# Kernel tuning notes

Measured on AMD Instinct MI355X. Metric: run time of the kernel, lower is better.

The kernel has to match this reference:

```python
import jax, jax.numpy as jnp
import numpy as np

B, C_L_IN, C_L_OUT, C_J = 512, 64, 64, 16


def setup_inputs() -> dict:
    key = jax.random.key(0)
    ks = jax.random.split(key, 8)
    std = 0.02 / C_L_IN ** 0.5
    return {
        "F_in": jax.random.normal(ks[0], (B, C_L_IN, 4, 4), jnp.float32),
        "theta": jax.random.normal(ks[1], (B, C_J), jnp.float32),
        "W_bias": std * jax.random.normal(ks[2], (C_L_OUT, C_L_IN, 4, 4), jnp.float32),
        "W_cos": std * jax.random.normal(ks[3], (C_L_OUT, C_L_IN, C_J, 4, 4), jnp.float32),
        "W_sin": std * jax.random.normal(ks[4], (C_L_OUT, C_L_IN, C_J, 4, 4), jnp.float32),
        "Wb_bias": std * jax.random.normal(ks[5], (C_L_OUT, C_L_IN, 4, 4), jnp.float32),
        "Wb_cos": std * jax.random.normal(ks[6], (C_L_OUT, C_L_IN, C_J, 4, 4), jnp.float32),
        "Wb_sin": std * jax.random.normal(ks[7], (C_L_OUT, C_L_IN, C_J, 4, 4), jnp.float32),
    }


def reference(F_in, theta, W_bias, W_cos, W_sin, Wb_bias, Wb_cos, Wb_sin):
    cos_t = jnp.cos(theta)  # (B, C_J)
    sin_t = jnp.sin(theta)
    # U, Ub: (B, C_L_out, C_L_in, 4, 4)
    U = (W_bias
         + jnp.einsum('jicpq,bc->bjipq', W_cos, cos_t)
         + jnp.einsum('jicpq,bc->bjipq', W_sin, sin_t))
    Ub = (Wb_bias
          + jnp.einsum('jicpq,bc->bjipq', Wb_cos, cos_t)
          + jnp.einsum('jicpq,bc->bjipq', Wb_sin, sin_t))
    term1 = jnp.einsum('bipq,bjiqr->bjpr', F_in, U)
    term2 = jnp.einsum('bjipq,biqr->bjpr', Ub, F_in)
    return term1 + term2
```

## Files before the change

### kernel.cpp

```cpp
#include <hip/hip_runtime.h>


#define NRO_B   512
#define NRO_CL  64
#define K_DIM   8448
#define M_DIM   2048
#define N_DIM   256
#define SK      8
#define B_ELems  ((size_t)N_DIM * K_DIM)
#define FV_ELems ((size_t)M_DIM * N_DIM)
#define P_ELems  ((size_t)2 * SK * M_DIM * N_DIM)

typedef __attribute__((ext_vector_type(8))) _Float16 half8;
typedef __attribute__((ext_vector_type(4))) _Float16 half4_t;
typedef __attribute__((ext_vector_type(4))) float floatx4;

__device__ __forceinline__ void load16(const float* p, float w[4][4]) {
    const float4* p4 = (const float4*)p;
    #pragma unroll
    for (int a = 0; a < 4; ++a) {
        float4 x = p4[a];
        w[a][0] = x.x; w[a][1] = x.y; w[a][2] = x.z; w[a][3] = x.w;
    }
}

__device__ __forceinline__ half8 scale8(half8 v, _Float16 s) {
    half8 r;
    #pragma unroll
    for (int x = 0; x < 8; ++x) r[x] = v[x] * s;
    return r;
}

__global__ __launch_bounds__(256) void nro_prep(
    const float* __restrict__ F_in,
    const float* __restrict__ W_bias, const float* __restrict__ W_cos,
    const float* __restrict__ W_sin,  const float* __restrict__ Wb_bias,
    const float* __restrict__ Wb_cos, const float* __restrict__ Wb_sin,
    _Float16* __restrict__ Bbuf,
    _Float16* __restrict__ Fv)
{
    const int w = threadIdx.x >> 6, i = threadIdx.x & 63;
    if (blockIdx.x < 128) {
        const int b = blockIdx.x * 4 + w;
        float f[4][4];
        load16(F_in + ((size_t)b * 64 + i) * 16, f);
        #pragma unroll
        for (int a = 0; a < 4; ++a) {
            half4_t v0 = { (_Float16)f[a][0], (_Float16)f[a][1],
                           (_Float16)f[a][2], (_Float16)f[a][3] };
            *(half4_t*)(Fv + (size_t)(b * 4 + a) * 256 + i * 4) = v0;
            half4_t v1 = { (_Float16)f[0][a], (_Float16)f[1][a],
                           (_Float16)f[2][a], (_Float16)f[3][a] };
            *(half4_t*)(Fv + FV_ELems + (size_t)(b * 4 + a) * 256 + i * 4) = v1;
        }
    } else {
        const int unit = (blockIdx.x - 128) * 4 + w;
        const int j = unit >> 5, c = (unit >> 1) & 15, h = unit & 1;
        _Float16* Bd = Bbuf + (size_t)h * B_ELems;
        const size_t wbase = (((size_t)(j * 64 + i)) * 16 + c) * 16;

        float wc4[4][4], ws4[4][4];
        if (h == 0) { load16(W_cos  + wbase, wc4); load16(W_sin  + wbase, ws4); }
        else        { load16(Wb_cos + wbase, wc4); load16(Wb_sin + wbase, ws4); }

        const int gc  = (1 + c)  * 8 + (i >> 3);
        const int gs  = (17 + c) * 8 + (i >> 3);
        const int kin = (i & 7) * 4;
        #pragma unroll
        for (int a = 0; a < 4; ++a) {
            const int n = j * 4 + a;
            half4_t vc, vs;
            if (h == 0) {
                vc = (half4_t){ (_Float16)wc4[0][a], (_Float16)wc4[1][a],
                                (_Float16)wc4[2][a], (_Float16)wc4[3][a] };
                vs = (half4_t){ (_Float16)ws4[0][a], (_Float16)ws4[1][a],
                                (_Float16)ws4[2][a], (_Float16)ws4[3][a] };
            } else {
                vc = (half4_t){ (_Float16)wc4[a][0], (_Float16)wc4[a][1],
                                (_Float16)wc4[a][2], (_Float16)wc4[a][3] };
                vs = (half4_t){ (_Float16)ws4[a][0], (_Float16)ws4[a][1],
                                (_Float16)ws4[a][2], (_Float16)ws4[a][3] };
            }
            *(half4_t*)(Bd + ((size_t)gc * 256 + n) * 32 + kin) = vc;
            *(half4_t*)(Bd + ((size_t)gs * 256 + n) * 32 + kin) = vs;
        }
        if (c == 0) {
            float t[4][4];
            load16(((h == 0) ? W_bias : Wb_bias) + ((size_t)(j * 64 + i)) * 16, t);
            #pragma unroll
            for (int a = 0; a < 4; ++a) {
                half4_t v;
                if (h == 0) v = (half4_t){ (_Float16)t[0][a], (_Float16)t[1][a],
                                           (_Float16)t[2][a], (_Float16)t[3][a] };
                else        v = (half4_t){ (_Float16)t[a][0], (_Float16)t[a][1],
                                           (_Float16)t[a][2], (_Float16)t[a][3] };
                *(half4_t*)(Bd + ((size_t)(i >> 3) * 256 + (j * 4 + a)) * 32 + kin) = v;
            }
        }
    }
}

__global__ __launch_bounds__(256, 2) void nro_gemm(
    const _Float16* __restrict__ Bbuf, const _Float16* __restrict__ Fv,
    const float* __restrict__ theta,
    float* __restrict__ part)
{
    const int zs = blockIdx.x;
    const int z  = zs >> 3;
    const int sk = zs & 7;
    const int m0 = blockIdx.y * 64;

    const _Float16* Bm = Bbuf + (size_t)z * B_ELems;
    const _Float16* Fm = Fv + (size_t)z * FV_ELems + (size_t)m0 * 256;

    __shared__ _Float16 Fs[64 * 264];
    __shared__ float    trig[16 * 34];

    const int tid  = threadIdx.x;
    const int lane = tid & 63;
    const int w    = tid >> 6;
    const int wn   = w * 64;

    #pragma unroll
    for (int kk = 0; kk < 8; ++kk) {
        const int idx = kk * 256 + tid;
        const int row = idx >> 5, cf = idx & 31;
        half8 v = *(const half8*)(Fm + (size_t)row * 256 + cf * 8);
        *(half8*)(Fs + row * 264 + cf * 8) = v;
    }
    {
        const int bl = tid >> 4, c = tid & 15;
        const float th = theta[(m0 >> 2) * 16 + tid];
        trig[bl * 34 + 1 + c]  = __cosf(th);
        trig[bl * 34 + 17 + c] = __sinf(th);
        if (c == 0) trig[bl * 34] = 1.0f;
    }
    __syncthreads();

    const int fr = lane & 15, fq8 = (lane >> 4) * 8;

    const _Float16* Brow[4];
    #pragma unroll
    for (int t = 0; t < 4; ++t)
        Brow[t] = Bm + (size_t)(wn + t * 16 + fr) * 32 + fq8;

    floatx4 acc[4][4] = {};
    _Float16 tv[4] = {};
    int cp_last = -1;

    const int base = sk * 33;
    half8 q0[4], q1[4];
    #pragma unroll
    for (int t = 0; t < 4; ++t) {
        q0[t] = *(const half8*)(Brow[t] + (size_t)(base + 0) * 8192);
        q1[t] = *(const half8*)(Brow[t] + (size_t)(base + 1) * 8192);
    }

    #define NRO_CHUNK(GABS, QREG)                                             \
        {                                                                     \
            const int cp_ = (GABS) >> 3;                                      \
            if (cp_ != cp_last) {                                             \
                cp_last = cp_;                                                \
                _Pragma("unroll")                                             \
                for (int t = 0; t < 4; ++t)                                   \
                    tv[t] = (_Float16)trig[(t * 4 + (fr >> 2)) * 34 + cp_];   \
            }                                                                 \
            const int iq0_ = ((GABS) & 7) * 32;                               \
            half8 af[4];                                                      \
            _Pragma("unroll")                                                 \
            for (int t = 0; t < 4; ++t) {                                     \
                half8 fvf = *(const half8*)(Fs + (t * 16 + fr) * 264          \
                                            + iq0_ + fq8);                    \
                af[t] = scale8(fvf, tv[t]);                                   \
            }                                                                 \
            _Pragma("unroll")                                                 \
            for (int mt = 0; mt < 4; ++mt)                                    \
                _Pragma("unroll")                                             \
                for (int nt = 0; nt < 4; ++nt)                                \
                    acc[mt][nt] = __builtin_amdgcn_mfma_f32_16x16x32_f16(     \
                        af[mt], QREG[nt], acc[mt][nt], 0, 0, 0);              \
        }

    for (int it = 0; it < 16; ++it) {
        const int c0 = base + 2 * it;
        half8 p0[4], p1[4];
        #pragma unroll
        for (int t = 0; t < 4; ++t)
            p0[t] = *(const half8*)(Brow[t] + (size_t)(c0 + 2) * 8192);
        if (it < 15) {
            #pragma unroll
            for (int t = 0; t < 4; ++t)
                p1[t] = *(const half8*)(Brow[t] + (size_t)(c0 + 3) * 8192);
        }
        NRO_CHUNK(c0, q0);
        NRO_CHUNK(c0 + 1, q1);
        #pragma unroll
        for (int t = 0; t < 4; ++t) q0[t] = p0[t];
        if (it < 15) {
            #pragma unroll
            for (int t = 0; t < 4; ++t) q1[t] = p1[t];
        }
    }
    NRO_CHUNK(base + 32, q0);
    #undef NRO_CHUNK

    const int col = lane & 15, row4 = (lane >> 4) * 4;
    #pragma unroll
    for (int mt = 0; mt < 4; ++mt)
        #pragma unroll
        for (int nt = 0; nt < 4; ++nt)
            #pragma unroll
            for (int e = 0; e < 4; ++e) {
                const int m = m0 + mt * 16 + row4 + e;
                const int n = wn + nt * 16 + col;
                part[((size_t)zs * M_DIM + m) * N_DIM + n] = acc[mt][nt][e];
            }
}

__global__ __launch_bounds__(256) void nro_reduce(
    const float* __restrict__ part, float* __restrict__ out)
{
    const int t = blockIdx.x * 256 + threadIdx.x;
    const int b = t >> 8;
    const int j = (t >> 2) & 63;
    const int p = t & 3;

    float4 o = make_float4(0.f, 0.f, 0.f, 0.f);
    #pragma unroll
    for (int sk = 0; sk < SK; ++sk) {
        const float4 c1 = *(const float4*)(
            part + ((size_t)sk * M_DIM + b * 4 + p) * N_DIM + j * 4);
        o.x += c1.x; o.y += c1.y; o.z += c1.z; o.w += c1.w;
        const float* p2 = part + ((size_t)(SK + sk) * M_DIM + b * 4) * N_DIM + j * 4 + p;
        o.x += p2[0 * N_DIM]; o.y += p2[1 * N_DIM];
        o.z += p2[2 * N_DIM]; o.w += p2[3 * N_DIM];
    }
    *(float4*)(out + ((size_t)(b * 64 + j) * 16 + p * 4)) = o;
}

__global__ __launch_bounds__(256, 2) void nro_fallback(
    const float* __restrict__ F_in, const float* __restrict__ theta,
    const float* __restrict__ W_bias, const float* __restrict__ W_cos,
    const float* __restrict__ W_sin,  const float* __restrict__ Wb_bias,
    const float* __restrict__ Wb_cos, const float* __restrict__ Wb_sin,
    float* __restrict__ out)
{
    __shared__ float smem[8448];
    const int j      = blockIdx.x >> 3;
    const int isplit = blockIdx.x & 7;
    const int i0     = isplit * 8;
    const int lane   = threadIdx.x & 63;
    const int chunk  = __builtin_amdgcn_readfirstlane(threadIdx.x >> 6);
    const int b      = blockIdx.y * 64 + lane;
    const int tid    = threadIdx.x;
    {
        float4* s4 = (float4*)smem;
        const int base16  = (j * 64 + i0) * 16;
        const int base256 = (j * 64 + i0) * 256;
        if (tid < 32)      s4[tid] = ((const float4*)(W_bias + base16))[tid];
        else if (tid < 64) s4[tid] = ((const float4*)(Wb_bias + base16))[tid - 32];
        #pragma unroll
        for (int r = 0; r < 2; ++r) {
            const int k = r * 256 + tid;
            s4[64 + k]   = ((const float4*)(W_cos  + base256))[k];
            s4[576 + k]  = ((const float4*)(W_sin  + base256))[k];
            s4[1088 + k] = ((const float4*)(Wb_cos + base256))[k];
            s4[1600 + k] = ((const float4*)(Wb_sin + base256))[k];
        }
    }
    float csc[16], css[16];
    #pragma unroll
    for (int c = 0; c < 16; ++c) {
        float t = theta[b * 16 + c];
        csc[c] = __cosf(t); css[c] = __sinf(t);
    }
    __syncthreads();
    float acc[16];
    #pragma unroll
    for (int e = 0; e < 16; ++e) acc[e] = 0.0f;
    #pragma unroll
    for (int ii = 0; ii < 2; ++ii) {
        const int il = chunk * 2 + ii;
        const int i  = i0 + il;
        float f[16];
        const float4* fp = (const float4*)(F_in + (b * 64 + i) * 16);
        #pragma unroll
        for (int v = 0; v < 4; ++v) {
            float4 x = fp[v];
            f[v*4+0]=x.x; f[v*4+1]=x.y; f[v*4+2]=x.z; f[v*4+3]=x.w;
        }
        const float* wb  = smem + il * 16;
        const float* wbb = smem + 128  + il * 16;
        const float* wc  = smem + 256  + il * 256;
        const float* wsn = smem + 2304 + il * 256;
        const float* wbc = smem + 4352 + il * 256;
        const float* wbs = smem + 6400 + il * 256;
        float U[16], Ub[16];
        #pragma unroll
        for (int e = 0; e < 16; ++e) { U[e] = wb[e]; Ub[e] = wbb[e]; }
        #pragma unroll 4
        for (int c = 0; c < 16; ++c) {
            const float cc = csc[c], ss = css[c];
            #pragma unroll
            for (int e = 0; e < 16; ++e) {
                U[e]  = fmaf(wc [c*16+e], cc, U[e]);
                U[e]  = fmaf(wsn[c*16+e], ss, U[e]);
                Ub[e] = fmaf(wbc[c*16+e], cc, Ub[e]);
                Ub[e] = fmaf(wbs[c*16+e], ss, Ub[e]);
            }
        }
        #pragma unroll
        for (int p = 0; p < 4; ++p)
            #pragma unroll
            for (int r = 0; r < 4; ++r) {
                float a = acc[p*4+r];
                #pragma unroll
                for (int q = 0; q < 4; ++q) {
                    a = fmaf(f[p*4+q],  U[q*4+r], a);
                    a = fmaf(Ub[p*4+q], f[q*4+r], a);
                }
                acc[p*4+r] = a;
            }
    }
    __syncthreads();
    if (chunk > 0) {
        float* r = smem + (chunk - 1) * 1088 + lane * 17;
        #pragma unroll
        for (int e = 0; e < 16; ++e) r[e] = acc[e];
    }
    __syncthreads();
    if (chunk == 0) {
        #pragma unroll
        for (int cc = 0; cc < 3; ++cc) {
            const float* r = smem + cc * 1088 + lane * 17;
            #pragma unroll
            for (int e = 0; e < 16; ++e) acc[e] += r[e];
        }
        float* o = out + ((size_t)b * 64 + j) * 16;
        #pragma unroll
        for (int e = 0; e < 16; ++e) atomicAdd(o + e, acc[e]);
    }
}

extern "C" void kernel_launch(void* const* d_in, const int* in_sizes, int n_in,
                              void* d_out, int out_size, void* d_ws, size_t ws_size,
                              hipStream_t stream) {
    const float* F_in    = (const float*)d_in[0];
    const float* theta   = (const float*)d_in[1];
    const float* W_bias  = (const float*)d_in[2];
    const float* W_cos   = (const float*)d_in[3];
    const float* W_sin   = (const float*)d_in[4];
    const float* Wb_bias = (const float*)d_in[5];
    const float* Wb_cos  = (const float*)d_in[6];
    const float* Wb_sin  = (const float*)d_in[7];
    float* out = (float*)d_out;

    const size_t needB  = 2 * B_ELems  * sizeof(_Float16);
    const size_t needFv = 2 * FV_ELems * sizeof(_Float16);
    const size_t needP  = P_ELems * sizeof(float);
    if (ws_size >= needB + needFv + needP) {
        _Float16* Bbuf = (_Float16*)d_ws;
        _Float16* Fv   = (_Float16*)((char*)d_ws + needB);
        float*    part = (float*)((char*)d_ws + needB + needFv);
        nro_prep<<<640, 256, 0, stream>>>(F_in, W_bias, W_cos, W_sin,
                                          Wb_bias, Wb_cos, Wb_sin, Bbuf, Fv);
        nro_gemm<<<dim3(16, 32), 256, 0, stream>>>(Bbuf, Fv, theta, part);
        nro_reduce<<<512, 256, 0, stream>>>(part, out);
    } else {
        hipMemsetAsync(out, 0, (size_t)out_size * sizeof(float), stream);
        dim3 grid(64 * 8, 512 / 64, 1);
        nro_fallback<<<grid, 256, 0, stream>>>(
            F_in, theta, W_bias, W_cos, W_sin, Wb_bias, Wb_cos, Wb_sin, out);
    }
}
```

Measured before the change: 110.2 us.

## Fuse split-K reduction into GEMM via last-block atomic counter

Removes the separate reduce kernel. Each GEMM block writes its partial tile, then bumps a per-row-block atomic counter, and the last of the 16 blocks sums all split-K partials and writes the output. The counters are zeroed in the prep kernel. This saves a kernel launch and lets the reduction overlap with other GEMM blocks, but the reduction now runs on only 32 blocks at the tail, which may serialize.

```diff
diff --git a/kernel.cpp b/kernel.cpp
--- a/kernel.cpp
+++ b/kernel.cpp
@@ -37,9 +37,11 @@
     const float* __restrict__ W_sin,  const float* __restrict__ Wb_bias,
     const float* __restrict__ Wb_cos, const float* __restrict__ Wb_sin,
     _Float16* __restrict__ Bbuf,
-    _Float16* __restrict__ Fv)
+    _Float16* __restrict__ Fv,
+    int* __restrict__ cnt)
 {
     const int w = threadIdx.x >> 6, i = threadIdx.x & 63;
+    if (blockIdx.x == 0 && threadIdx.x < 32) cnt[threadIdx.x] = 0;
     if (blockIdx.x < 128) {
         const int b = blockIdx.x * 4 + w;
         float f[4][4];
@@ -103,7 +105,9 @@
 __global__ __launch_bounds__(256, 2) void nro_gemm(
     const _Float16* __restrict__ Bbuf, const _Float16* __restrict__ Fv,
     const float* __restrict__ theta,
-    float* __restrict__ part)
+    float* __restrict__ part,
+    int* __restrict__ cnt,
+    float* __restrict__ out)
 {
     const int zs = blockIdx.x;
     const int z  = zs >> 3;
@@ -115,6 +119,7 @@
 
     __shared__ _Float16 Fs[64 * 264];
     __shared__ float    trig[16 * 34];
+    __shared__ int      s_old;
 
     const int tid  = threadIdx.x;
     const int lane = tid & 63;
@@ -204,38 +209,48 @@
     NRO_CHUNK(base + 32, q0);
     #undef NRO_CHUNK
 
-    const int col = lane & 15, row4 = (lane >> 4) * 4;
-    #pragma unroll
-    for (int mt = 0; mt < 4; ++mt)
-        #pragma unroll
-        for (int nt = 0; nt < 4; ++nt)
-            #pragma unroll
-            for (int e = 0; e < 4; ++e) {
-                const int m = m0 + mt * 16 + row4 + e;
-                const int n = wn + nt * 16 + col;
-                part[((size_t)zs * M_DIM + m) * N_DIM + n] = acc[mt][nt][e];
-            }
-}
-
-__global__ __launch_bounds__(256) void nro_reduce(
-    const float* __restrict__ part, float* __restrict__ out)
-{
-    const int t = blockIdx.x * 256 + threadIdx.x;
-    const int b = t >> 8;
-    const int j = (t >> 2) & 63;
-    const int p = t & 3;
-
-    float4 o = make_float4(0.f, 0.f, 0.f, 0.f);
-    #pragma unroll
-    for (int sk = 0; sk < SK; ++sk) {
-        const float4 c1 = *(const float4*)(
-            part + ((size_t)sk * M_DIM + b * 4 + p) * N_DIM + j * 4);
-        o.x += c1.x; o.y += c1.y; o.z += c1.z; o.w += c1.w;
-        const float* p2 = part + ((size_t)(SK + sk) * M_DIM + b * 4) * N_DIM + j * 4 + p;
-        o.x += p2[0 * N_DIM]; o.y += p2[1 * N_DIM];
-        o.z += p2[2 * N_DIM]; o.w += p2[3 * N_DIM];
-    }
-    *(float4*)(out + ((size_t)(b * 64 + j) * 16 + p * 4)) = o;
+    {
+        const int col = lane & 15, row4 = (lane >> 4) * 4;
+        #pragma unroll
+        for (int mt = 0; mt < 4; ++mt)
+            #pragma unroll
+            for (int nt = 0; nt < 4; ++nt)
+                #pragma unroll
+                for (int e = 0; e < 4; ++e) {
+                    const int m = m0 + mt * 16 + row4 + e;
+                    const int n = wn + nt * 16 + col;
+                    part[((size_t)zs * M_DIM + m) * N_DIM + n] = acc[mt][nt][e];
+                }
+    }
+
+    __threadfence();
+    __syncthreads();
+    if (tid == 0) s_old = atomicAdd(&cnt[blockIdx.y], 1);
+    __syncthreads();
+    if (s_old == 15) {
+        __threadfence();
+        const int b0 = blockIdx.y * 16;
+        #pragma unroll 4
+        for (int u = 0; u < 16; ++u) {
+            const int idx = u * 256 + tid;
+            const int bl  = idx >> 8;
+            const int j   = (idx >> 2) & 63;
+            const int p   = idx & 3;
+            const int b   = b0 + bl;
+
+            float4 o = make_float4(0.f, 0.f, 0.f, 0.f);
+            #pragma unroll
+            for (int s = 0; s < SK; ++s) {
+                const float4 c1 = *(const float4*)(
+                    part + ((size_t)s * M_DIM + b * 4 + p) * N_DIM + j * 4);
+                o.x += c1.x; o.y += c1.y; o.z += c1.z; o.w += c1.w;
+                const float* p2 = part + ((size_t)(SK + s) * M_DIM + b * 4) * N_DIM + j * 4 + p;
+                o.x += p2[0 * N_DIM]; o.y += p2[1 * N_DIM];
+                o.z += p2[2 * N_DIM]; o.w += p2[3 * N_DIM];
+            }
+            *(float4*)(out + ((size_t)(b * 64 + j) * 16 + p * 4)) = o;
+        }
+    }
 }
 
 __global__ __launch_bounds__(256, 2) void nro_fallback(
@@ -358,14 +373,15 @@
     const size_t needB  = 2 * B_ELems  * sizeof(_Float16);
     const size_t needFv = 2 * FV_ELems * sizeof(_Float16);
     const size_t needP  = P_ELems * sizeof(float);
-    if (ws_size >= needB + needFv + needP) {
+    const size_t needC  = 32 * sizeof(int);
+    if (ws_size >= needB + needFv + needP + needC) {
         _Float16* Bbuf = (_Float16*)d_ws;
         _Float16* Fv   = (_Float16*)((char*)d_ws + needB);
         float*    part = (float*)((char*)d_ws + needB + needFv);
+        int*      cnt  = (int*)((char*)d_ws + needB + needFv + needP);
         nro_prep<<<640, 256, 0, stream>>>(F_in, W_bias, W_cos, W_sin,
-                                          Wb_bias, Wb_cos, Wb_sin, Bbuf, Fv);
-        nro_gemm<<<dim3(16, 32), 256, 0, stream>>>(Bbuf, Fv, theta, part);
-        nro_reduce<<<512, 256, 0, stream>>>(part, out);
+                                          Wb_bias, Wb_cos, Wb_sin, Bbuf, Fv, cnt);
+        nro_gemm<<<dim3(16, 32), 256, 0, stream>>>(Bbuf, Fv, theta, part, cnt, out);
     } else {
         hipMemsetAsync(out, 0, (size_t)out_size * sizeof(float), stream);
         dim3 grid(64 * 8, 512 / 64, 1);
```

New measurement: 282.2 us. +156.0%, slower.
